# Optimization experiments

Measured on AMD Instinct MI355X. Metric: run time of the kernel, lower is better.

Reference implementation:

```python
import jax, jax.numpy as jnp
import numpy as np
from jax import lax

B, N, C_IN, C_OUT = 16, 4096, 64, 128
NPOINT, K = 1024, 16
EPS = 1e-5


def farthest_point_sample(p, npoint):
    # p: [B,N,3] -> indices [B,npoint]; deterministic start at index 0
    b, n, _ = p.shape

    def step(carry, _):
        distance, farthest = carry  # [B,N], [B]
        centroid = jnp.take_along_axis(p, farthest[:, None, None], axis=1)  # [B,1,3]
        dist = jnp.sum((p - centroid) ** 2, axis=-1)  # [B,N]
        distance = jnp.minimum(distance, dist)
        new_far = jnp.argmax(distance, axis=-1).astype(jnp.int32)
        return (distance, new_far), farthest

    init = (jnp.full((b, n), 1e10, dtype=p.dtype), jnp.zeros((b,), jnp.int32))
    _, idx = lax.scan(step, init, None, length=npoint)  # [npoint,B]
    return idx.T  # [B,npoint]


def setup_inputs() -> dict:
    key = jax.random.key(0)
    k1, k2, k3 = jax.random.split(key, 3)
    return {
        "x": jax.random.normal(k1, (B, N, C_IN), dtype=jnp.float32),
        "p": jax.random.uniform(k2, (B, N, 3), dtype=jnp.float32),
        "conv_w": jax.random.normal(k3, (C_OUT, C_IN), dtype=jnp.float32) * 0.05,
        "gamma": jnp.ones((C_OUT,), jnp.float32),
        "beta": jnp.zeros((C_OUT,), jnp.float32),
    }


def reference(x, p, conv_w, gamma, beta):
    idx = farthest_point_sample(lax.stop_gradient(p), NPOINT)  # [B,npoint]
    new_x0 = jnp.take_along_axis(x, idx[..., None], axis=1)  # [B,npoint,C_in]
    new_p = jnp.take_along_axis(p, idx[..., None], axis=1)   # [B,npoint,3]
    # dense pairwise squared distance [B,npoint,N]
    dist = jnp.sum((new_p[:, :, None, :] - p[:, None, :, :]) ** 2, axis=-1)
    # k+1 smallest, drop self (distance 0) like argsort()[...,1:k+1]
    _, knn_idx = lax.top_k(-dist, K + 1)
    knn_idx = knn_idx[..., 1:]  # [B,npoint,K]
    flat = knn_idx.reshape(B, -1)  # [B,npoint*K]
    feature = jnp.take_along_axis(x, flat[..., None], axis=1).reshape(B, NPOINT, K, C_IN)
    diff = new_x0[:, :, None, :] - feature  # [B,npoint,K,C_in]
    # Conv1d(kernel_size=1, bias=False)
    h = jnp.einsum("bnkc,oc->bnko", diff, conv_w)  # [B,npoint,K,C_out]
    # BatchNorm1d (training mode -> batch stats over B and length dims)
    mean = jnp.mean(h, axis=(0, 1, 2))
    var = jnp.var(h, axis=(0, 1, 2))
    h = (h - mean) * lax.rsqrt(var + EPS) * gamma + beta
    h = jax.nn.relu(h)
    out = jnp.max(h, axis=2)  # max over K neighbors -> [B,npoint,C_out]
    return out, new_p
```

## Files before the change

kernel.cpp:

```cpp
#include <hip/hip_runtime.h>

#define B_   16
#define N_   4096
#define CIN  64
#define COUT 128
#define NPT  1024
#define KNNK 16

typedef unsigned long long u64;

__device__ __forceinline__ float fINF() { return __int_as_float(0x7f800000); }

template<int CTRL>
__device__ __forceinline__ float fmax_dpp(float v) {
    int x = __builtin_amdgcn_update_dpp(0, __float_as_int(v), CTRL, 0xF, 0xF, true);
    return fmaxf(v, __int_as_float(x));
}
template<int CTRL>
__device__ __forceinline__ float fmin_dpp(float v) {
    int x = __builtin_amdgcn_update_dpp(0, __float_as_int(v), CTRL, 0xF, 0xF, true);
    return fminf(v, __int_as_float(x));
}
template<int CTRL>
__device__ __forceinline__ u64 u64min_dpp(u64 k) {
    unsigned lo = (unsigned)k, hi = (unsigned)(k >> 32);
    unsigned plo = (unsigned)__builtin_amdgcn_update_dpp(0, (int)lo, CTRL, 0xF, 0xF, true);
    unsigned phi = (unsigned)__builtin_amdgcn_update_dpp(0, (int)hi, CTRL, 0xF, 0xF, true);
    u64 pk = ((u64)phi << 32) | plo;
    return pk < k ? pk : k;
}

__global__ __launch_bounds__(1024) void fps_kernel(const float* __restrict__ p,
                                                   int* __restrict__ idx_out,
                                                   float* __restrict__ newp_out) {
    __shared__ float  sval[2][16];
    __shared__ float4 sres[2];
    __shared__ int    sidx[NPT];

    const int b = blockIdx.x;
    const int t = threadIdx.x;
    const int lane = t & 63, wave = t >> 6;
    const float* pb = p + (size_t)b * N_ * 3;

    const float4* pb4 = (const float4*)pb;
    float4 a0 = pb4[t * 3 + 0], a1 = pb4[t * 3 + 1], a2 = pb4[t * 3 + 2];
    float lx[4], ly[4], lz[4], dist[4];
    lx[0] = a0.x; ly[0] = a0.y; lz[0] = a0.z;
    lx[1] = a0.w; ly[1] = a1.x; lz[1] = a1.y;
    lx[2] = a1.z; ly[2] = a1.w; lz[2] = a2.x;
    lx[3] = a2.y; ly[3] = a2.z; lz[3] = a2.w;
    dist[0] = dist[1] = dist[2] = dist[3] = 1e10f;

    float cx = pb[0], cy = pb[1], cz = pb[2];
    if (t == 0) sidx[0] = 0;

    for (int s = 1; s < NPT; ++s) {
        const int par = s & 1;
        float nd0, nd1, nd2, nd3;
        {
            float dx, dy, dz, d;
            dx = lx[0]-cx; dy = ly[0]-cy; dz = lz[0]-cz; d = dx*dx + dy*dy + dz*dz;
            nd0 = fminf(dist[0], d); dist[0] = nd0;
            dx = lx[1]-cx; dy = ly[1]-cy; dz = lz[1]-cz; d = dx*dx + dy*dy + dz*dz;
            nd1 = fminf(dist[1], d); dist[1] = nd1;
            dx = lx[2]-cx; dy = ly[2]-cy; dz = lz[2]-cz; d = dx*dx + dy*dy + dz*dz;
            nd2 = fminf(dist[2], d); dist[2] = nd2;
            dx = lx[3]-cx; dy = ly[3]-cy; dz = lz[3]-cz; d = dx*dx + dy*dy + dz*dz;
            nd3 = fminf(dist[3], d); dist[3] = nd3;
        }
        float bv = fmaxf(fmaxf(nd0, nd1), fmaxf(nd2, nd3));
        bv = fmax_dpp<0xB1>(bv);
        bv = fmax_dpp<0x4E>(bv);
        bv = fmax_dpp<0x141>(bv);
        bv = fmax_dpp<0x140>(bv);
        bv = fmaxf(bv, __shfl_xor(bv, 16));
        bv = fmaxf(bv, __shfl_xor(bv, 32));
        if (lane == 0) sval[par][wave] = bv;
        __syncthreads();
        float v = sval[par][lane & 15];
        float gmax = v;
        gmax = fmax_dpp<0xB1>(gmax);
        gmax = fmax_dpp<0x4E>(gmax);
        gmax = fmax_dpp<0x141>(gmax);
        gmax = fmax_dpp<0x140>(gmax);
        u64 ball = __ballot(v == gmax);
        int wwave = (int)__builtin_ctzll(ball);
        if (wave == wwave) {
            bool m = (nd0 == bv) | (nd1 == bv) | (nd2 == bv) | (nd3 == bv);
            u64 b2 = __ballot(m);
            int winlane = (int)__builtin_ctzll(b2);
            if (lane == winlane) {
                int j = (nd0 == bv) ? 0 : ((nd1 == bv) ? 1 : ((nd2 == bv) ? 2 : 3));
                float wx = (j == 0) ? lx[0] : (j == 1) ? lx[1] : (j == 2) ? lx[2] : lx[3];
                float wy = (j == 0) ? ly[0] : (j == 1) ? ly[1] : (j == 2) ? ly[2] : ly[3];
                float wz = (j == 0) ? lz[0] : (j == 1) ? lz[1] : (j == 2) ? lz[2] : lz[3];
                float4 r; r.x = wx; r.y = wy; r.z = wz; r.w = __int_as_float(t * 4 + j);
                sres[par] = r;
            }
        }
        __syncthreads();
        float4 r = sres[par];
        cx = r.x; cy = r.y; cz = r.z;
        if (t == 0) sidx[s] = __float_as_int(r.w);
    }
    __syncthreads();

    {
        int i = sidx[t];
        idx_out[b * NPT + t] = i;
        float* np = newp_out + ((size_t)b * NPT + t) * 3;
        np[0] = pb[3 * i + 0]; np[1] = pb[3 * i + 1]; np[2] = pb[3 * i + 2];
    }
}

__global__ __launch_bounds__(256) void knn_kernel(const float* __restrict__ p,
                                                  const int* __restrict__ idx_in,
                                                  int* __restrict__ knn_out) {
    __shared__ u64 skey[2][4];

    const int blk = blockIdx.x;
    const int b = blk >> 10, n = blk & 1023;
    const int t = threadIdx.x;
    const int lane = t & 63, wave = t >> 6;
    const float* pb = p + (size_t)b * N_ * 3;

    const int qi = idx_in[b * NPT + n];
    const float qx = pb[qi * 3 + 0], qy = pb[qi * 3 + 1], qz = pb[qi * 3 + 2];

    float fl[48];
    const float4* pb4 = (const float4*)pb;
#pragma unroll
    for (int i = 0; i < 12; ++i) {
        float4 v = pb4[t * 12 + i];
        fl[4 * i + 0] = v.x; fl[4 * i + 1] = v.y; fl[4 * i + 2] = v.z; fl[4 * i + 3] = v.w;
    }
    float dist[16];
#pragma unroll
    for (int j = 0; j < 16; ++j) {
        float dx = fl[3 * j + 0] - qx;
        float dy = fl[3 * j + 1] - qy;
        float dz = fl[3 * j + 2] - qz;
        dist[j] = dx * dx + dy * dy + dz * dz;
    }

    float lmin;
    {
        float m0 = fminf(fminf(dist[0], dist[1]), fminf(dist[2], dist[3]));
        float m1 = fminf(fminf(dist[4], dist[5]), fminf(dist[6], dist[7]));
        float m2 = fminf(fminf(dist[8], dist[9]), fminf(dist[10], dist[11]));
        float m3 = fminf(fminf(dist[12], dist[13]), fminf(dist[14], dist[15]));
        lmin = fminf(fminf(m0, m1), fminf(m2, m3));
    }

    int* kout = knn_out + ((size_t)b * NPT + n) * KNNK;

    for (int r = 0; r < 17; ++r) {
        const int par = r & 1;
        float wv = lmin;
        wv = fmin_dpp<0xB1>(wv);
        wv = fmin_dpp<0x4E>(wv);
        wv = fmin_dpp<0x141>(wv);
        wv = fmin_dpp<0x140>(wv);
        wv = fminf(wv, __shfl_xor(wv, 16));
        wv = fminf(wv, __shfl_xor(wv, 32));
        u64 ball = __ballot(lmin == wv);
        int winlane = (int)__builtin_ctzll(ball);
        if (lane == winlane) {
            int j = 15;
#pragma unroll
            for (int jj = 15; jj >= 0; --jj)
                if (dist[jj] == wv) j = jj;
            skey[par][wave] = ((u64)__float_as_uint(wv) << 32) | (unsigned)(t * 16 + j);
        }
        __syncthreads();
        u64 k = skey[par][lane & 3];
        k = u64min_dpp<0xB1>(k);
        k = u64min_dpp<0x4E>(k);
        const int widx = (int)(unsigned)(k & 0xFFFFFFFFull);
        if (t == 0 && r > 0) kout[r - 1] = widx;
        if ((widx >> 10) == wave) {
            if ((widx >> 4) == t) {
#pragma unroll
                for (int jj = 0; jj < 16; ++jj)
                    if ((widx & 15) == jj) dist[jj] = fINF();
                float m0 = fminf(fminf(dist[0], dist[1]), fminf(dist[2], dist[3]));
                float m1 = fminf(fminf(dist[4], dist[5]), fminf(dist[6], dist[7]));
                float m2 = fminf(fminf(dist[8], dist[9]), fminf(dist[10], dist[11]));
                float m3 = fminf(fminf(dist[12], dist[13]), fminf(dist[14], dist[15]));
                lmin = fminf(fminf(m0, m1), fminf(m2, m3));
            }
        }
    }
}

__global__ __launch_bounds__(256) void stats_kernel(const float* __restrict__ x,
                                                    const int* __restrict__ idx_in,
                                                    const int* __restrict__ knn_in,
                                                    float* __restrict__ part) {
    __shared__ float xc[4 * 64];
    __shared__ float dls[64 * 72];

    const int blk = blockIdx.x;
    const int t = threadIdx.x;
    const int q0 = blk * 64;
    const int b = q0 >> 10;
    const float* xb = x + (size_t)b * N_ * CIN;

    float acc[4][4];
#pragma unroll
    for (int i = 0; i < 4; ++i)
#pragma unroll
        for (int j = 0; j < 4; ++j) acc[i][j] = 0.f;
    float dsum = 0.f;

    const int r0 = (t >> 4) * 4, c0 = (t & 15) * 4;

    for (int sg = 0; sg < 16; ++sg) {
        __syncthreads();
        {
            int qq = t >> 6, c = t & 63;
            int q = q0 + sg * 4 + qq;
            int ci = idx_in[q];
            xc[qq * 64 + c] = xb[ci * CIN + c];
        }
        __syncthreads();
        for (int i = 0; i < 16; ++i) {
            int f = t + 256 * i;
            int qq = f >> 10, k = (f >> 6) & 15, c = f & 63;
            int q = q0 + sg * 4 + qq;
            int row = knn_in[q * KNNK + k];
            dls[(qq * 16 + k) * 72 + c] = xc[qq * 64 + c] - xb[row * CIN + c];
        }
        __syncthreads();
#pragma unroll 4
        for (int s = 0; s < 64; ++s) {
            const float4 a  = *(const float4*)&dls[s * 72 + r0];
            const float4 bb = *(const float4*)&dls[s * 72 + c0];
            acc[0][0] += a.x * bb.x; acc[0][1] += a.x * bb.y; acc[0][2] += a.x * bb.z; acc[0][3] += a.x * bb.w;
            acc[1][0] += a.y * bb.x; acc[1][1] += a.y * bb.y; acc[1][2] += a.y * bb.z; acc[1][3] += a.y * bb.w;
            acc[2][0] += a.z * bb.x; acc[2][1] += a.z * bb.y; acc[2][2] += a.z * bb.z; acc[2][3] += a.z * bb.w;
            acc[3][0] += a.w * bb.x; acc[3][1] += a.w * bb.y; acc[3][2] += a.w * bb.z; acc[3][3] += a.w * bb.w;
        }
        if (t < 64) {
            for (int s = 0; s < 64; ++s) dsum += dls[s * 72 + t];
        }
    }

    float* pout = part + (size_t)blk * 4160;
#pragma unroll
    for (int i = 0; i < 4; ++i)
#pragma unroll
        for (int j = 0; j < 4; ++j)
            pout[(r0 + i) * 64 + (c0 + j)] = acc[i][j];
    if (t < 64) pout[4096 + t] = dsum;
}

__global__ __launch_bounds__(256) void reduce_kernel(const float* __restrict__ part,
                                                     float* __restrict__ M) {
    int e = blockIdx.x * 256 + threadIdx.x;
    if (e >= 4160) return;
    float s = 0.f;
    for (int b = 0; b < 256; ++b) s += part[(size_t)b * 4160 + e];
    M[e] = s;
}

__global__ __launch_bounds__(64) void scale_kernel(const float* __restrict__ M,
                                                   const float* __restrict__ w,
                                                   const float* __restrict__ gamma,
                                                   const float* __restrict__ beta,
                                                   float* __restrict__ st) {
    __shared__ float wv[64];
    const int o = blockIdx.x, t = threadIdx.x;
    wv[t] = w[o * 64 + t];
    __syncthreads();
    const float* Mr = M + t * 64;
    float sr = 0.f;
    for (int c = 0; c < 64; ++c) sr += Mr[c] * wv[c];
    float e2 = wv[t] * sr;
    float mn = wv[t] * M[4096 + t];
#pragma unroll
    for (int off = 32; off >= 1; off >>= 1) {
        e2 += __shfl_xor(e2, off);
        mn += __shfl_xor(mn, off);
    }
    if (t == 0) {
        const float Ns = 262144.0f;
        float mean = mn / Ns;
        float var = e2 / Ns - mean * mean;
        float scale = gamma[o] * rsqrtf(var + 1e-5f);
        st[o] = scale;
        st[128 + o] = beta[o] - mean * scale;
    }
}

__global__ __launch_bounds__(256) void out_kernel(const float* __restrict__ x,
                                                  const float* __restrict__ w,
                                                  const int* __restrict__ idx_in,
                                                  const int* __restrict__ knn_in,
                                                  const float* __restrict__ st,
                                                  float* __restrict__ out) {
    __shared__ float wT[64 * 132];
    __shared__ float ss[256];
    __shared__ float df4[16 * 260];
    __shared__ int   skr[64];
    __shared__ int   sci[4];

    const int blk = blockIdx.x;
    const int b = blk >> 8, n0 = (blk & 255) * 4;
    const int t = threadIdx.x;
    const float* xb = x + (size_t)b * N_ * CIN;

    for (int i = 0; i < 32; ++i) {
        int f = t + 256 * i;
        int o = f >> 6, c = f & 63;
        wT[c * 132 + o] = w[f];
    }
    ss[t] = st[t];
    if (t < 64) skr[t] = knn_in[((size_t)b * NPT + n0) * KNNK + t];
    if (t < 4)  sci[t] = idx_in[b * NPT + n0 + t];
    __syncthreads();

    for (int i = 0; i < 16; ++i) {
        int c = t >> 2, q = t & 3;
        int center = sci[q];
        int row = skr[q * 16 + i];
        df4[i * 260 + c * 4 + q] = xb[center * CIN + c] - xb[row * CIN + c];
    }
    __syncthreads();

    const int k = t & 15, oq = t >> 4;
    float acc[4][8];
#pragma unroll
    for (int q = 0; q < 4; ++q)
#pragma unroll
        for (int i = 0; i < 8; ++i) acc[q][i] = 0.f;

    const float* dr = &df4[k * 260];
    for (int c = 0; c < 64; ++c) {
        const float4 d4 = *(const float4*)&dr[c * 4];
        const float4 w0 = *(const float4*)&wT[c * 132 + oq * 8 + 0];
        const float4 w1 = *(const float4*)&wT[c * 132 + oq * 8 + 4];
        float dv[4] = {d4.x, d4.y, d4.z, d4.w};
        float wvv[8] = {w0.x, w0.y, w0.z, w0.w, w1.x, w1.y, w1.z, w1.w};
#pragma unroll
        for (int q = 0; q < 4; ++q)
#pragma unroll
            for (int i = 0; i < 8; ++i) acc[q][i] += dv[q] * wvv[i];
    }

#pragma unroll
    for (int q = 0; q < 4; ++q)
#pragma unroll
        for (int i = 0; i < 8; ++i) {
            int o = oq * 8 + i;
            float v = fmaxf(acc[q][i] * ss[o] + ss[128 + o], 0.f);
            v = fmax_dpp<0xB1>(v);
            v = fmax_dpp<0x4E>(v);
            v = fmax_dpp<0x141>(v);
            v = fmax_dpp<0x140>(v);
            acc[q][i] = v;
        }
    if (k == 0) {
#pragma unroll
        for (int q = 0; q < 4; ++q) {
            float4 o0 = {acc[q][0], acc[q][1], acc[q][2], acc[q][3]};
            float4 o1 = {acc[q][4], acc[q][5], acc[q][6], acc[q][7]};
            float* op = out + ((size_t)b * NPT + n0 + q) * COUT + oq * 8;
            *(float4*)&op[0] = o0;
            *(float4*)&op[4] = o1;
        }
    }
}

extern "C" void kernel_launch(void* const* d_in, const int* in_sizes, int n_in,
                              void* d_out, int out_size, void* d_ws, size_t ws_size,
                              hipStream_t stream) {
    const float* x     = (const float*)d_in[0];
    const float* p     = (const float*)d_in[1];
    const float* w     = (const float*)d_in[2];
    const float* gamma = (const float*)d_in[3];
    const float* beta  = (const float*)d_in[4];

    float* out  = (float*)d_out;
    float* newp = out + (size_t)B_ * NPT * COUT;

    char* ws = (char*)d_ws;
    int*   idx  = (int*)(ws + 0);
    int*   knn  = (int*)(ws + 65536);
    float* part = (float*)(ws + 1114112);
    float* M    = (float*)(ws + 5373952);
    float* st   = (float*)(ws + 5390592);

    hipLaunchKernelGGL(fps_kernel,   dim3(B_),          dim3(1024), 0, stream, p, idx, newp);
    hipLaunchKernelGGL(knn_kernel,   dim3(B_ * NPT),    dim3(256),  0, stream, p, idx, knn);
    hipLaunchKernelGGL(stats_kernel, dim3(256),         dim3(256),  0, stream, x, idx, knn, part);
    hipLaunchKernelGGL(reduce_kernel,dim3(17),          dim3(256),  0, stream, part, M);
    hipLaunchKernelGGL(scale_kernel, dim3(128),         dim3(64),   0, stream, M, w, gamma, beta, st);
    hipLaunchKernelGGL(out_kernel,   dim3(B_ * NPT/4),  dim3(256),  0, stream, x, w, idx, knn, st, out);
}
```

Baseline: 1.136 ms.

## Cut FPS to one barrier per step with packed per-wave argmax keys

The farthest-point-sampling loop now runs 512 threads with 8 points each. Each wave writes a packed (max distance, index) key to LDS, and every thread then reduces the 8 keys after a single barrier. The winner's coordinates are read from an LDS copy of the whole cloud, which removes the second barrier and the winner-broadcast step from each of the 1023 serial iterations. The KNN kernel's 64-bit min reduction is replaced by a float min, ballot and shuffle. The cost is more LDS (48KB for coordinates) and more registers per thread.

```diff
diff --git a/kernel.cpp b/kernel.cpp
--- a/kernel.cpp
+++ b/kernel.cpp
@@ -21,95 +21,94 @@
     int x = __builtin_amdgcn_update_dpp(0, __float_as_int(v), CTRL, 0xF, 0xF, true);
     return fminf(v, __int_as_float(x));
 }
-template<int CTRL>
-__device__ __forceinline__ u64 u64min_dpp(u64 k) {
-    unsigned lo = (unsigned)k, hi = (unsigned)(k >> 32);
-    unsigned plo = (unsigned)__builtin_amdgcn_update_dpp(0, (int)lo, CTRL, 0xF, 0xF, true);
-    unsigned phi = (unsigned)__builtin_amdgcn_update_dpp(0, (int)hi, CTRL, 0xF, 0xF, true);
-    u64 pk = ((u64)phi << 32) | plo;
-    return pk < k ? pk : k;
-}
-
-__global__ __launch_bounds__(1024) void fps_kernel(const float* __restrict__ p,
-                                                   int* __restrict__ idx_out,
-                                                   float* __restrict__ newp_out) {
-    __shared__ float  sval[2][16];
-    __shared__ float4 sres[2];
-    __shared__ int    sidx[NPT];
+
+__global__ __launch_bounds__(512) void fps_kernel(const float* __restrict__ p,
+                                                  int* __restrict__ idx_out,
+                                                  float* __restrict__ newp_out) {
+    __shared__ float sx[N_], sy[N_], sz[N_];
+    __shared__ int   sidx[NPT];
+    __shared__ u64   slot[2][8];
 
     const int b = blockIdx.x;
     const int t = threadIdx.x;
-    const int lane = t & 63, wave = t >> 6;
+    const int lane = t & 63;
+    const int wave = t >> 6;
     const float* pb = p + (size_t)b * N_ * 3;
 
+    for (int i = 0; i < 24; ++i) {
+        int f = t + 512 * i;
+        float v = pb[f];
+        int pt = f / 3, c = f - pt * 3;
+        if (c == 0) sx[pt] = v; else if (c == 1) sy[pt] = v; else sz[pt] = v;
+    }
+
     const float4* pb4 = (const float4*)pb;
-    float4 a0 = pb4[t * 3 + 0], a1 = pb4[t * 3 + 1], a2 = pb4[t * 3 + 2];
-    float lx[4], ly[4], lz[4], dist[4];
-    lx[0] = a0.x; ly[0] = a0.y; lz[0] = a0.z;
-    lx[1] = a0.w; ly[1] = a1.x; lz[1] = a1.y;
-    lx[2] = a1.z; ly[2] = a1.w; lz[2] = a2.x;
-    lx[3] = a2.y; ly[3] = a2.z; lz[3] = a2.w;
-    dist[0] = dist[1] = dist[2] = dist[3] = 1e10f;
+    float4 a0 = pb4[6*t+0], a1 = pb4[6*t+1], a2 = pb4[6*t+2];
+    float4 a3 = pb4[6*t+3], a4 = pb4[6*t+4], a5 = pb4[6*t+5];
+    float lx[8], ly[8], lz[8], dist[8];
+    lx[0]=a0.x; ly[0]=a0.y; lz[0]=a0.z;
+    lx[1]=a0.w; ly[1]=a1.x; lz[1]=a1.y;
+    lx[2]=a1.z; ly[2]=a1.w; lz[2]=a2.x;
+    lx[3]=a2.y; ly[3]=a2.z; lz[3]=a2.w;
+    lx[4]=a3.x; ly[4]=a3.y; lz[4]=a3.z;
+    lx[5]=a3.w; ly[5]=a4.x; lz[5]=a4.y;
+    lx[6]=a4.z; ly[6]=a4.w; lz[6]=a5.x;
+    lx[7]=a5.y; ly[7]=a5.z; lz[7]=a5.w;
+#pragma unroll
+    for (int j = 0; j < 8; ++j) dist[j] = 1e10f;
 
     float cx = pb[0], cy = pb[1], cz = pb[2];
     if (t == 0) sidx[0] = 0;
 
     for (int s = 1; s < NPT; ++s) {
         const int par = s & 1;
-        float nd0, nd1, nd2, nd3;
-        {
-            float dx, dy, dz, d;
-            dx = lx[0]-cx; dy = ly[0]-cy; dz = lz[0]-cz; d = dx*dx + dy*dy + dz*dz;
-            nd0 = fminf(dist[0], d); dist[0] = nd0;
-            dx = lx[1]-cx; dy = ly[1]-cy; dz = lz[1]-cz; d = dx*dx + dy*dy + dz*dz;
-            nd1 = fminf(dist[1], d); dist[1] = nd1;
-            dx = lx[2]-cx; dy = ly[2]-cy; dz = lz[2]-cz; d = dx*dx + dy*dy + dz*dz;
-            nd2 = fminf(dist[2], d); dist[2] = nd2;
-            dx = lx[3]-cx; dy = ly[3]-cy; dz = lz[3]-cz; d = dx*dx + dy*dy + dz*dz;
-            nd3 = fminf(dist[3], d); dist[3] = nd3;
-        }
-        float bv = fmaxf(fmaxf(nd0, nd1), fmaxf(nd2, nd3));
+        float nd[8];
+#pragma unroll
+        for (int j = 0; j < 8; ++j) {
+            float dx = lx[j]-cx, dy = ly[j]-cy, dz = lz[j]-cz;
+            float d = dx*dx + dy*dy + dz*dz;
+            nd[j] = fminf(dist[j], d);
+            dist[j] = nd[j];
+        }
+        float lmax = fmaxf(fmaxf(fmaxf(nd[0],nd[1]), fmaxf(nd[2],nd[3])),
+                           fmaxf(fmaxf(nd[4],nd[5]), fmaxf(nd[6],nd[7])));
+        float bv = lmax;
         bv = fmax_dpp<0xB1>(bv);
         bv = fmax_dpp<0x4E>(bv);
         bv = fmax_dpp<0x141>(bv);
         bv = fmax_dpp<0x140>(bv);
         bv = fmaxf(bv, __shfl_xor(bv, 16));
         bv = fmaxf(bv, __shfl_xor(bv, 32));
-        if (lane == 0) sval[par][wave] = bv;
+        u64 ball = __ballot(lmax == bv);
+        int winlane = (int)__builtin_ctzll(ball);
+        if (lane == winlane) {
+            int cj = 7;
+#pragma unroll
+            for (int jj = 7; jj >= 0; --jj)
+                if (nd[jj] == bv) cj = jj;
+            slot[par][wave] = ((u64)__float_as_uint(bv) << 32)
+                            | (unsigned)(t * 8 + cj);
+        }
         __syncthreads();
-        float v = sval[par][lane & 15];
+        u64 k = slot[par][lane & 7];
+        float v = __uint_as_float((unsigned)(k >> 32));
         float gmax = v;
         gmax = fmax_dpp<0xB1>(gmax);
         gmax = fmax_dpp<0x4E>(gmax);
         gmax = fmax_dpp<0x141>(gmax);
-        gmax = fmax_dpp<0x140>(gmax);
-        u64 ball = __ballot(v == gmax);
-        int wwave = (int)__builtin_ctzll(ball);
-        if (wave == wwave) {
-            bool m = (nd0 == bv) | (nd1 == bv) | (nd2 == bv) | (nd3 == bv);
-            u64 b2 = __ballot(m);
-            int winlane = (int)__builtin_ctzll(b2);
-            if (lane == winlane) {
-                int j = (nd0 == bv) ? 0 : ((nd1 == bv) ? 1 : ((nd2 == bv) ? 2 : 3));
-                float wx = (j == 0) ? lx[0] : (j == 1) ? lx[1] : (j == 2) ? lx[2] : lx[3];
-                float wy = (j == 0) ? ly[0] : (j == 1) ? ly[1] : (j == 2) ? ly[2] : ly[3];
-                float wz = (j == 0) ? lz[0] : (j == 1) ? lz[1] : (j == 2) ? lz[2] : lz[3];
-                float4 r; r.x = wx; r.y = wy; r.z = wz; r.w = __int_as_float(t * 4 + j);
-                sres[par] = r;
-            }
-        }
-        __syncthreads();
-        float4 r = sres[par];
-        cx = r.x; cy = r.y; cz = r.z;
-        if (t == 0) sidx[s] = __float_as_int(r.w);
+        u64 b2 = __ballot(v == gmax);
+        int winslot = (int)__builtin_ctzll(b2);
+        int widx = __shfl((int)(unsigned)(k & 0xFFFFFFFFull), winslot);
+        cx = sx[widx]; cy = sy[widx]; cz = sz[widx];
+        if (t == 0) sidx[s] = widx;
     }
     __syncthreads();
 
-    {
-        int i = sidx[t];
-        idx_out[b * NPT + t] = i;
-        float* np = newp_out + ((size_t)b * NPT + t) * 3;
-        np[0] = pb[3 * i + 0]; np[1] = pb[3 * i + 1]; np[2] = pb[3 * i + 2];
+    for (int s2 = t; s2 < NPT; s2 += 512) {
+        int i = sidx[s2];
+        idx_out[b * NPT + s2] = i;
+        float* np = newp_out + ((size_t)b * NPT + s2) * 3;
+        np[0] = sx[i]; np[1] = sy[i]; np[2] = sz[i];
     }
 }
 
@@ -174,9 +173,13 @@
         }
         __syncthreads();
         u64 k = skey[par][lane & 3];
-        k = u64min_dpp<0xB1>(k);
-        k = u64min_dpp<0x4E>(k);
-        const int widx = (int)(unsigned)(k & 0xFFFFFFFFull);
+        float v = __uint_as_float((unsigned)(k >> 32));
+        float gmin = v;
+        gmin = fmin_dpp<0xB1>(gmin);
+        gmin = fmin_dpp<0x4E>(gmin);
+        u64 b2 = __ballot(v == gmin);
+        int winslot = (int)__builtin_ctzll(b2);
+        const int widx = __shfl((int)(unsigned)(k & 0xFFFFFFFFull), winslot);
         if (t == 0 && r > 0) kout[r - 1] = widx;
         if ((widx >> 10) == wave) {
             if ((widx >> 4) == t) {
@@ -391,7 +394,7 @@
     float* M    = (float*)(ws + 5373952);
     float* st   = (float*)(ws + 5390592);
 
-    hipLaunchKernelGGL(fps_kernel,   dim3(B_),          dim3(1024), 0, stream, p, idx, newp);
+    hipLaunchKernelGGL(fps_kernel,   dim3(B_),          dim3(512),  0, stream, p, idx, newp);
     hipLaunchKernelGGL(knn_kernel,   dim3(B_ * NPT),    dim3(256),  0, stream, p, idx, knn);
     hipLaunchKernelGGL(stats_kernel, dim3(256),         dim3(256),  0, stream, x, idx, knn, part);
     hipLaunchKernelGGL(reduce_kernel,dim3(17),          dim3(256),  0, stream, part, M);
```

New measurement: 1.051 ms. -7.4%, faster.
